# Optimization experiments

Measured on AMD Instinct MI355X. Metric: run time of the kernel, lower is better.

The kernel has to match this reference:

```python
import jax, jax.numpy as jnp
import numpy as np

A2B = 1.8897259886          # angstrom -> bohr
EV2HA = 0.0367493
NUM_RBF = 16
R_MIN = 0.5 * A2B
R_MAX = 4.0 * A2B           # r_max_angstroms=4.0 from gnn_config
RBF_WIDTH = (R_MAX - R_MIN) / NUM_RBF
N_NODES = 100_000
N_EDGES = 3_200_000
EMBED_DIM = 16
N_ELEMS = 4
CODES_PER_ELEM = 4          # all elements are core -> max_codes_per_element
TOTAL_CODES = N_ELEMS * CODES_PER_ELEM
NUM_PAIRS = 10
CODE_OWNER = np.repeat(np.arange(N_ELEMS), CODES_PER_ELEM)  # element owning each code


def setup_inputs() -> dict:
    key = jax.random.key(0)
    ks = jax.random.split(key, 12)
    N, E, D = N_NODES, N_EDGES, EMBED_DIM
    inv_sp = lambda v: np.float32(np.log(np.expm1(v)))  # inverse_softplus
    return {
        "elem_idx": jax.random.randint(ks[0], (N,), 0, N_ELEMS),
        "edge_index": jax.random.randint(ks[1], (2, E), 0, N),
        "distances": jax.random.uniform(ks[2], (E,), minval=1.0, maxval=7.5),  # bohr
        "pair_idx": jax.random.randint(ks[3], (E,), 0, NUM_PAIRS),
        "embed": jax.random.normal(ks[4], (N_ELEMS, D)),
        "fw1": jax.random.normal(ks[5], (D, NUM_RBF)) * 0.3,
        "fb1": jnp.zeros((D,)),
        "fw2": jax.random.normal(ks[6], (D, D)) * 0.3,
        "fb2": jnp.zeros((D,)),
        "mw1": jax.random.normal(ks[7], (D, D)) * 0.3,
        "mb1": jnp.zeros((D,)),
        "mw2": jax.random.normal(ks[8], (3, D)) * 0.05,  # zero-init in orig; small random for a live baseline
        "mb2": jnp.zeros((3,)),
        "codebook": jax.random.normal(ks[9], (TOTAL_CODES, D)),
        "raw_D_e": jnp.full((NUM_PAIRS,), inv_sp(0.1 * EV2HA)),
        "raw_alpha": jnp.full((NUM_PAIRS,), inv_sp(1.5 / A2B)),
        "raw_r0": jnp.full((NUM_PAIRS,), np.float32(3.0 * A2B)),
    }


def reference(elem_idx, edge_index, distances, pair_idx, embed,
              fw1, fb1, fw2, fb2, mw1, mb1, mw2, mb2,
              codebook, raw_D_e, raw_alpha, raw_r0):
    # --- EnvironmentEncoder: gather + edge filter + scatter_add ---
    h = embed[elem_idx]                                              # [N, D]
    centers = jnp.linspace(R_MIN, R_MAX, NUM_RBF, dtype=distances.dtype)
    rbf = jnp.exp(-0.5 * ((distances[:, None] - centers) / RBF_WIDTH) ** 2)  # [E, RBF]
    W = jax.nn.silu(rbf @ fw1.T + fb1) @ fw2.T + fb2                 # [E, D]
    src, tgt = edge_index[0], edge_index[1]
    messages = h[tgt] * W                                            # [E, D]
    agg = jax.ops.segment_sum(messages, src, num_segments=h.shape[0])
    h = h + agg                                                      # [N, D]

    # --- VectorQuantizer (eval path): per-element masked cdist + argmin ---
    d2 = (jnp.sum(h * h, axis=1, keepdims=True)
          - 2.0 * h @ codebook.T
          + jnp.sum(codebook * codebook, axis=1))                    # [N, C] squared dist
    owner = jnp.asarray(CODE_OWNER)
    valid = elem_idx[:, None] == owner[None, :]                      # [N, C]
    atom_types = jnp.argmin(jnp.where(valid, d2, jnp.inf), axis=1)   # [N]
    z_q = codebook[atom_types]                                       # [N, D]
    h_q = h + jax.lax.stop_gradient(z_q - h)                         # straight-through
    # all elements have >1 code -> commitment over all atoms
    vq_loss = 0.25 * jnp.mean((h - jax.lax.stop_gradient(z_q)) ** 2)

    # --- MorseParameterPredictor: edge gather + MLP ---
    pair_feat = h_q[src] + h_q[tgt]                                  # [E, D]
    delta = jax.nn.silu(pair_feat @ mw1.T + mb1) @ mw2.T + mb2       # [E, 3]

    D_e = jax.nn.softplus(raw_D_e[pair_idx] + delta[:, 0])
    alpha = jax.nn.softplus(raw_alpha[pair_idx] + delta[:, 1])
    r0 = raw_r0[pair_idx] + delta[:, 2]
    params = jnp.stack([D_e, alpha, r0], axis=-1)                    # [E, 3]
    return params, vq_loss
```

## Files before the change

### kernel.cpp

```cpp
#include <hip/hip_runtime.h>
#include <stdint.h>

#define A2B   1.8897259886f
#define R_MIN (0.5f * A2B)
#define R_MAX (4.0f * A2B)

#define EPB   2048
#define CSH   9

__global__ void __launch_bounds__(256) k_bucket(
        const int* __restrict__ src, const int* __restrict__ tgt,
        const int* __restrict__ elem, const float* __restrict__ dist,
        int* __restrict__ gCursor, float* __restrict__ dBuf,
        unsigned short* __restrict__ kBuf, int CAP, int E)
{
    __shared__ int cnt[4][256], sbase[4][256];
    int t = threadIdx.x;
    int w = t >> 6;
    cnt[0][t] = 0; cnt[1][t] = 0; cnt[2][t] = 0; cnt[3][t] = 0;
    __syncthreads();
    int e0 = blockIdx.x * EPB;
    int eEnd = (e0 + EPB < E) ? e0 + EPB : E;

    float dv[8]; int bv[8]; unsigned short kv[8];
    #pragma unroll
    for (int j = 0; j < 8; ++j) {
        int e = e0 + t + j * 256;
        if (e < eEnd) {
            int s = src[e];
            int q = elem[tgt[e]];
            dv[j] = dist[e];
            int b = s >> CSH;
            bv[j] = b;
            kv[j] = (unsigned short)(((s - (b << CSH)) << 2) | q);
            atomicAdd(&cnt[w][b], 1);
        }
    }
    __syncthreads();
    {
        int c0 = cnt[0][t], c1 = cnt[1][t], c2 = cnt[2][t], c3 = cnt[3][t];
        int tot = c0 + c1 + c2 + c3;
        int g = (tot > 0) ? atomicAdd(&gCursor[t], tot) : 0;
        sbase[0][t] = g;
        sbase[1][t] = g + c0;
        sbase[2][t] = g + c0 + c1;
        sbase[3][t] = g + c0 + c1 + c2;
        cnt[0][t] = 0; cnt[1][t] = 0; cnt[2][t] = 0; cnt[3][t] = 0;
    }
    __syncthreads();
    #pragma unroll
    for (int j = 0; j < 8; ++j) {
        int e = e0 + t + j * 256;
        if (e < eEnd) {
            int b = bv[j];
            int pos = sbase[w][b] + atomicAdd(&cnt[w][b], 1);
            if (pos < CAP) {
                size_t idx = (size_t)b * CAP + pos;
                dBuf[idx] = dv[j];
                kBuf[idx] = kv[j];
            }
        }
    }
}

__global__ void __launch_bounds__(256) k_bscan(
        const int* __restrict__ gCursor, int* __restrict__ bucketBase,
        int* __restrict__ offs, const float* __restrict__ fw1,
        float* __restrict__ fw1t, int NBUK, int N, int E)
{
    __shared__ int sd[256];
    int t = threadIdx.x;
    fw1t[t] = fw1[(t & 15) * 16 + (t >> 4)];
    int v = (t < NBUK) ? gCursor[t] : 0;
    sd[t] = v; __syncthreads();
    #pragma unroll
    for (int o = 1; o < 256; o <<= 1) {
        int x = (t >= o) ? sd[t - o] : 0;
        __syncthreads();
        sd[t] += x;
        __syncthreads();
    }
    bucketBase[t] = sd[t] - v;
    if (t == 0) offs[N] = E;
}

__global__ void __launch_bounds__(256) k_bin(
        const float* __restrict__ dBuf, const unsigned short* __restrict__ kBuf,
        const int* __restrict__ gCursor, const int* __restrict__ bucketBase,
        int* __restrict__ offs, float* __restrict__ payload,
        int CAP, int N)
{
    __shared__ int lcnt[512];
    __shared__ int sd[256];
    int t = threadIdx.x;
    int cb = blockIdx.x >> 2, fc = blockIdx.x & 3;
    int n0 = cb << CSH;
    int n1 = n0 + (1 << CSH); if (n1 > N) n1 = N;
    int m  = n1 - n0;
    int cntE = gCursor[cb]; if (cntE > CAP) cntE = CAP;
    int base = bucketBase[cb];
    lcnt[t] = 0; lcnt[t + 256] = 0;
    __syncthreads();
    const float* dB = dBuf + (size_t)cb * CAP;
    const unsigned short* kB = kBuf + (size_t)cb * CAP;
    for (int i = t; i < cntE; i += 256)
        atomicAdd(&lcnt[kB[i] >> 2], 1);
    __syncthreads();
    int b2 = t * 2;
    int v0 = (b2 < m)     ? lcnt[b2]     : 0;
    int v1 = (b2 + 1 < m) ? lcnt[b2 + 1] : 0;
    int tsum = v0 + v1;
    sd[t] = tsum; __syncthreads();
    #pragma unroll
    for (int o = 1; o < 256; o <<= 1) {
        int x = (t >= o) ? sd[t - o] : 0;
        __syncthreads();
        sd[t] += x;
        __syncthreads();
    }
    int run = sd[t] - tsum;
    if (b2 < m) {
        if ((b2 >> 7) == fc) offs[n0 + b2] = base + run;
        lcnt[b2] = run; run += v0;
    }
    if (b2 + 1 < m) {
        if (((b2 + 1) >> 7) == fc) offs[n0 + b2 + 1] = base + run;
        lcnt[b2 + 1] = run;
    }
    __syncthreads();
    for (int i = t; i < cntE; i += 256) {
        int kv = kB[i];
        int l = kv >> 2;
        if ((l >> 7) == fc) {
            int pos = atomicAdd(&lcnt[l], 1);
            unsigned db = __float_as_uint(dB[i]);
            payload[base + pos] = __uint_as_float((db & ~3u) | (unsigned)(kv & 3));
        }
    }
}

__global__ void __launch_bounds__(256) k_gather(
        const int* __restrict__ elem, const float* __restrict__ embed,
        const float* __restrict__ codebook,
        const float4* __restrict__ fw1t4, const float* __restrict__ fb1,
        const float* __restrict__ fw2, const float* __restrict__ fb2,
        const int* __restrict__ offs, const float* __restrict__ payload,
        int* __restrict__ atype, float* __restrict__ loss, int N)
{
    __shared__ float4 s_fw2v[64];
    __shared__ float s_cb[256];
    __shared__ float s_fb1[16], s_fb2[16], s_emb[64], s_cbn[16];
    __shared__ float s_red[4];
    __shared__ int s_ord[64];
    int t = threadIdx.x;
    {
        float* f2 = (float*)s_fw2v;
        f2[t] = fw2[t];
        s_cb[t] = codebook[t];
    }
    if (t < 16) { s_fb1[t] = fb1[t]; s_fb2[t] = fb2[t]; }
    if (t < 64) s_emb[t] = embed[t];
    int nbase = blockIdx.x * 64;
    if (t < 64) {
        int n = nbase + t;
        int dg = (n < N) ? (offs[n + 1] - offs[n]) : 0x7FFF;
        s_ord[t] = (dg << 6) | t;
    }
    __syncthreads();
    if (t < 16) {
        float s = 0.f;
        #pragma unroll
        for (int j = 0; j < 16; ++j) { float c = s_cb[t * 16 + j]; s += c * c; }
        s_cbn[t] = s;
    }
    for (int ksz = 2; ksz <= 64; ksz <<= 1) {
        for (int jj = ksz >> 1; jj > 0; jj >>= 1) {
            __syncthreads();
            if (t < 64) {
                int ixj = t ^ jj;
                if (ixj > t) {
                    int a = s_ord[t], b = s_ord[ixj];
                    bool asc = ((t & ksz) == 0);
                    if (asc ? (a > b) : (a < b)) { s_ord[t] = b; s_ord[ixj] = a; }
                }
            }
        }
    }
    __syncthreads();

    int node = nbase + (s_ord[t >> 2] & 63);
    int sub  = t & 3;
    float lp = 0.0f;
    if (node < N) {
        int o0 = offs[node], o1 = offs[node + 1];
        float G0[16], G1[16], G2[16], G3[16];
        #pragma unroll
        for (int j = 0; j < 16; ++j) { G0[j]=0.f; G1[j]=0.f; G2[j]=0.f; G3[j]=0.f; }
        float c0 = 0.f, c1 = 0.f, c2 = 0.f, c3 = 0.f;

        const float invw   = 16.0f / (R_MAX - R_MIN);
        const float u0base = R_MIN * invw;
        const float kstep  = 16.0f / 15.0f;
        for (int i = o0 + sub; i < o1; i += 8) {
            int ii = i + 4;
            bool has2 = (ii < o1);
            unsigned p0 = __float_as_uint(payload[i]);
            unsigned p1 = has2 ? __float_as_uint(payload[ii]) : p0;
            int q0 = (int)(p0 & 3u), q1 = (int)(p1 & 3u);
            float d0 = __uint_as_float(p0 & ~3u);
            float d1 = __uint_as_float(p1 & ~3u);
            float ua = d0 * invw - u0base;
            float ub = d1 * invw - u0base;
            float g0[16], g1[16];
            #pragma unroll
            for (int i2 = 0; i2 < 16; ++i2) { g0[i2] = s_fb1[i2]; g1[i2] = s_fb1[i2]; }
            #pragma clang loop unroll(disable)
            for (int k = 0; k < 16; ++k) {
                float r0 = __expf(-0.5f * ua * ua);
                float r1 = __expf(-0.5f * ub * ub);
                float4 w0 = fw1t4[k*4+0], w1 = fw1t4[k*4+1];
                float4 w2 = fw1t4[k*4+2], w3 = fw1t4[k*4+3];
                g0[0]+=r0*w0.x;  g0[1]+=r0*w0.y;  g0[2]+=r0*w0.z;  g0[3]+=r0*w0.w;
                g0[4]+=r0*w1.x;  g0[5]+=r0*w1.y;  g0[6]+=r0*w1.z;  g0[7]+=r0*w1.w;
                g0[8]+=r0*w2.x;  g0[9]+=r0*w2.y;  g0[10]+=r0*w2.z; g0[11]+=r0*w2.w;
                g0[12]+=r0*w3.x; g0[13]+=r0*w3.y; g0[14]+=r0*w3.z; g0[15]+=r0*w3.w;
                g1[0]+=r1*w0.x;  g1[1]+=r1*w0.y;  g1[2]+=r1*w0.z;  g1[3]+=r1*w0.w;
                g1[4]+=r1*w1.x;  g1[5]+=r1*w1.y;  g1[6]+=r1*w1.z;  g1[7]+=r1*w1.w;
                g1[8]+=r1*w2.x;  g1[9]+=r1*w2.y;  g1[10]+=r1*w2.z; g1[11]+=r1*w2.w;
                g1[12]+=r1*w3.x; g1[13]+=r1*w3.y; g1[14]+=r1*w3.z; g1[15]+=r1*w3.w;
                ua -= kstep; ub -= kstep;
            }
            {
                float m0 = (q0==0)?1.f:0.f, m1 = (q0==1)?1.f:0.f;
                float m2 = (q0==2)?1.f:0.f, m3 = (q0==3)?1.f:0.f;
                c0 += m0; c1 += m1; c2 += m2; c3 += m3;
                #pragma unroll
                for (int i2 = 0; i2 < 16; ++i2) {
                    float a = g0[i2];
                    float s = a * __builtin_amdgcn_rcpf(1.0f + __expf(-a));
                    G0[i2] += m0*s; G1[i2] += m1*s; G2[i2] += m2*s; G3[i2] += m3*s;
                }
            }
            if (has2) {
                float m0 = (q1==0)?1.f:0.f, m1 = (q1==1)?1.f:0.f;
                float m2 = (q1==2)?1.f:0.f, m3 = (q1==3)?1.f:0.f;
                c0 += m0; c1 += m1; c2 += m2; c3 += m3;
                #pragma unroll
                for (int i2 = 0; i2 < 16; ++i2) {
                    float a = g1[i2];
                    float s = a * __builtin_amdgcn_rcpf(1.0f + __expf(-a));
                    G0[i2] += m0*s; G1[i2] += m1*s; G2[i2] += m2*s; G3[i2] += m3*s;
                }
            }
        }
        #pragma unroll
        for (int mm = 1; mm <= 2; mm <<= 1) {
            #pragma unroll
            for (int j = 0; j < 16; ++j) {
                G0[j] += __shfl_xor(G0[j], mm, 64);
                G1[j] += __shfl_xor(G1[j], mm, 64);
                G2[j] += __shfl_xor(G2[j], mm, 64);
                G3[j] += __shfl_xor(G3[j], mm, 64);
            }
            c0 += __shfl_xor(c0, mm, 64);
            c1 += __shfl_xor(c1, mm, 64);
            c2 += __shfl_xor(c2, mm, 64);
            c3 += __shfl_xor(c3, mm, 64);
        }
        float Gs[16];
        #pragma unroll
        for (int j = 0; j < 16; ++j)
            Gs[j] = (sub==0) ? G0[j] : (sub==1) ? G1[j] : (sub==2) ? G2[j] : G3[j];
        float cs = (sub==0) ? c0 : (sub==1) ? c1 : (sub==2) ? c2 : c3;
        const float* er = s_emb + sub * 16;
        float acc[16];
        #pragma clang loop unroll_count(4)
        for (int j = 0; j < 16; ++j) {
            float4 f0 = s_fw2v[j*4+0], f1 = s_fw2v[j*4+1];
            float4 f2 = s_fw2v[j*4+2], f3 = s_fw2v[j*4+3];
            float w = Gs[0]*f0.x  + Gs[1]*f0.y  + Gs[2]*f0.z  + Gs[3]*f0.w
                    + Gs[4]*f1.x  + Gs[5]*f1.y  + Gs[6]*f1.z  + Gs[7]*f1.w
                    + Gs[8]*f2.x  + Gs[9]*f2.y  + Gs[10]*f2.z + Gs[11]*f2.w
                    + Gs[12]*f3.x + Gs[13]*f3.y + Gs[14]*f3.z + Gs[15]*f3.w;
            acc[j] = (w + cs * s_fb2[j]) * er[j];
        }
        #pragma unroll
        for (int mm = 1; mm <= 2; mm <<= 1) {
            #pragma unroll
            for (int j = 0; j < 16; ++j)
                acc[j] += __shfl_xor(acc[j], mm, 64);
        }
        int qn = elem[node];
        float h[16], hh = 0.f;
        #pragma unroll
        for (int j = 0; j < 16; ++j) {
            h[j] = acc[j] + s_emb[qn * 16 + j];
            hh += h[j] * h[j];
        }
        float best = __builtin_inff(); int bi = 0;
        #pragma unroll
        for (int c = 0; c < 4; ++c) {
            int code = qn * 4 + c;
            float dot = 0.f;
            #pragma unroll
            for (int j = 0; j < 16; ++j) dot += h[j] * s_cb[code * 16 + j];
            float d2 = hh - 2.0f * dot + s_cbn[code];
            if (d2 < best) { best = d2; bi = code; }
        }
        if (sub == 0) {
            atype[node] = bi;
            #pragma unroll
            for (int j = 0; j < 16; ++j) {
                float df = h[j] - s_cb[bi * 16 + j];
                lp += df * df;
            }
        }
    }
    #pragma unroll
    for (int o = 32; o > 0; o >>= 1) lp += __shfl_down(lp, o, 64);
    int wid = t >> 6;
    if ((t & 63) == 0) s_red[wid] = lp;
    __syncthreads();
    if (t == 0) atomicAdd(loss, s_red[0] + s_red[1] + s_red[2] + s_red[3]);
}

__global__ void __launch_bounds__(256) k_table(
        const float* __restrict__ codebook,
        const float* __restrict__ mw1, const float* __restrict__ mb1,
        const float* __restrict__ mw2, const float* __restrict__ mb2,
        const float* __restrict__ rD, const float* __restrict__ rA,
        const float* __restrict__ rR,
        const float* __restrict__ loss, float4* __restrict__ table,
        float* __restrict__ out_loss, float inv_nd)
{
    __shared__ float s_cb[256], s_mw1[256], s_mb1[16], s_mw2[48], s_mb2[3];
    __shared__ float s_rd[10], s_ra[10], s_rr[10];
    int tid = threadIdx.x;
    s_cb[tid] = codebook[tid];
    s_mw1[tid] = mw1[tid];
    if (tid < 16) s_mb1[tid] = mb1[tid];
    if (tid < 48) s_mw2[tid] = mw2[tid];
    if (tid < 3)  s_mb2[tid] = mb2[tid];
    if (tid < 10) { s_rd[tid] = rD[tid]; s_ra[tid] = rA[tid]; s_rr[tid] = rR[tid]; }
    __syncthreads();

    int a = tid >> 4, b = tid & 15;
    float pf[16];
    #pragma unroll
    for (int j = 0; j < 16; ++j) pf[j] = s_cb[a * 16 + j] + s_cb[b * 16 + j];
    float hid[16];
    #pragma unroll
    for (int i = 0; i < 16; ++i) {
        float acc = s_mb1[i];
        #pragma unroll
        for (int j = 0; j < 16; ++j) acc += pf[j] * s_mw1[i * 16 + j];
        hid[i] = acc / (1.0f + __expf(-acc));
    }
    float del[3];
    #pragma unroll
    for (int r = 0; r < 3; ++r) {
        float acc = s_mb2[r];
        #pragma unroll
        for (int i = 0; i < 16; ++i) acc += hid[i] * s_mw2[r * 16 + i];
        del[r] = acc;
    }
    #pragma unroll
    for (int p = 0; p < 10; ++p) {
        float xd = s_rd[p] + del[0];
        float xa = s_ra[p] + del[1];
        float De = (xd > 20.f) ? xd : log1pf(__expf(xd));
        float al = (xa > 20.f) ? xa : log1pf(__expf(xa));
        float r0 = s_rr[p] + del[2];
        table[tid * 10 + p] = make_float4(De, al, r0, 0.f);
    }
    if (tid == 0) out_loss[0] = 0.25f * loss[0] * inv_nd;
}

__global__ void __launch_bounds__(256) k_out(
        const int* __restrict__ src, const int* __restrict__ tgt,
        const int* __restrict__ pidx, const int* __restrict__ atype,
        const float4* __restrict__ table, float2* __restrict__ out, int Ehalf)
{
    int i = blockIdx.x * 256 + threadIdx.x;
    if (i >= Ehalf) return;
    int2 s2 = ((const int2*)src)[i];
    int2 t2 = ((const int2*)tgt)[i];
    int2 p2 = ((const int2*)pidx)[i];
    int i0 = (atype[s2.x] * 16 + atype[t2.x]) * 10 + p2.x;
    int i1 = (atype[s2.y] * 16 + atype[t2.y]) * 10 + p2.y;
    float4 t0 = table[i0];
    float4 t1 = table[i1];
    float2* op = out + (size_t)3 * i;
    op[0] = make_float2(t0.x, t0.y);
    op[1] = make_float2(t0.z, t1.x);
    op[2] = make_float2(t1.y, t1.z);
}

extern "C" void kernel_launch(void* const* d_in, const int* in_sizes, int n_in,
                              void* d_out, int out_size, void* d_ws, size_t ws_size,
                              hipStream_t stream)
{
    (void)n_in;
    const int*   elem  = (const int*)d_in[0];
    const int*   eidx  = (const int*)d_in[1];
    const float* dist  = (const float*)d_in[2];
    const int*   pidx  = (const int*)d_in[3];
    const float* embed = (const float*)d_in[4];
    const float* fw1   = (const float*)d_in[5];
    const float* fb1   = (const float*)d_in[6];
    const float* fw2   = (const float*)d_in[7];
    const float* fb2   = (const float*)d_in[8];
    const float* mw1   = (const float*)d_in[9];
    const float* mb1   = (const float*)d_in[10];
    const float* mw2   = (const float*)d_in[11];
    const float* mb2   = (const float*)d_in[12];
    const float* cb    = (const float*)d_in[13];
    const float* rD    = (const float*)d_in[14];
    const float* rA    = (const float*)d_in[15];
    const float* rR    = (const float*)d_in[16];

    int N = in_sizes[0];
    int E = in_sizes[2];
    const int* src = eidx;
    const int* tgt = eidx + E;

    int NBUK = (N + (1 << CSH) - 1) >> CSH;
    if (NBUK > 256) return;
    long long expv = ((long long)E << CSH) / N;
    int CAP = (int)(expv + expv / 16 + 256);

    size_t outBytes = (size_t)out_size * 4;
    char* ob = (char*)d_out;
    size_t oc = 0;
    float* dBuf = (float*)(ob + oc);           oc += (size_t)NBUK * CAP * 4;
    unsigned short* kBuf = (unsigned short*)(ob + oc); oc += (size_t)NBUK * CAP * 2;
    oc = (oc + 3) & ~(size_t)3;
    float* payload = (float*)(ob + oc);        oc += (size_t)E * 4;
    int*   offs    = (int*)(ob + oc);          oc += (size_t)(N + 1) * 4;
    if (oc > outBytes) return;

    char* ws = (char*)d_ws;
    size_t cur = 0;
    int*   gCursor    = (int*)(ws + cur);  cur += 256 * 4;
    float* loss       = (float*)(ws + cur); cur += 4;
    size_t clearB = cur;
    cur = (cur + 15) & ~(size_t)15;
    int*   bucketBase = (int*)(ws + cur);  cur += 256 * 4;
    float* fw1t       = (float*)(ws + cur); cur += 256 * 4;
    int*   atype      = (int*)(ws + cur);  cur += (size_t)N * 4;
    cur = (cur + 15) & ~(size_t)15;
    float4* table     = (float4*)(ws + cur); cur += 2560 * sizeof(float4);
    if (ws_size < cur) return;

    hipMemsetAsync(d_ws, 0, clearB, stream);

    k_bucket<<<(E + EPB - 1) / EPB, 256, 0, stream>>>(
        src, tgt, elem, dist, gCursor, dBuf, kBuf, CAP, E);
    k_bscan<<<1, 256, 0, stream>>>(gCursor, bucketBase, offs, fw1, fw1t,
                                   NBUK, N, E);
    k_bin<<<NBUK * 4, 256, 0, stream>>>(dBuf, kBuf, gCursor, bucketBase,
                                        offs, payload, CAP, N);
    k_gather<<<(N + 63) / 64, 256, 0, stream>>>(elem, embed, cb,
                                                (const float4*)fw1t, fb1,
                                                fw2, fb2, offs, payload,
                                                atype, loss, N);
    float* outl = (float*)d_out + (size_t)3 * E;
    k_table<<<1, 256, 0, stream>>>(cb, mw1, mb1, mw2, mb2, rD, rA, rR,
                                   loss, table, outl,
                                   1.0f / (float)((size_t)N * 16));
    k_out<<<(E / 2 + 255) / 256, 256, 0, stream>>>(src, tgt, pidx, atype, table,
                                                   (float2*)d_out, E / 2);
}
```

Before: 263.8 us.

## Fold bucket scan into binning kernel and quantize edge-filter accumulators to integers

Removes the single-block scan kernel: the weight transpose moves into the bucketing kernel, and each binning block recomputes the bucket prefix sum itself. Binning now uses two blocks per bucket instead of four. The gather kernel accumulates SiLU outputs as fixed-point integers with select-add instead of float mask multiplies. The goal is fewer launches and cheaper masked accumulation, at the cost of quantization error and redundant scans.

```diff
diff --git a/kernel.cpp b/kernel.cpp
--- a/kernel.cpp
+++ b/kernel.cpp
@@ -7,16 +7,21 @@
 
 #define EPB   2048
 #define CSH   9
+#define QSCALE 1048576.0f
+#define QINV   (1.0f / 1048576.0f)
 
 __global__ void __launch_bounds__(256) k_bucket(
         const int* __restrict__ src, const int* __restrict__ tgt,
         const int* __restrict__ elem, const float* __restrict__ dist,
+        const float* __restrict__ fw1, float* __restrict__ fw1t,
         int* __restrict__ gCursor, float* __restrict__ dBuf,
         unsigned short* __restrict__ kBuf, int CAP, int E)
 {
     __shared__ int cnt[4][256], sbase[4][256];
     int t = threadIdx.x;
     int w = t >> 6;
+    if (blockIdx.x == 0)
+        fw1t[t] = fw1[(t & 15) * 16 + (t >> 4)];
     cnt[0][t] = 0; cnt[1][t] = 0; cnt[2][t] = 0; cnt[3][t] = 0;
     __syncthreads();
     int e0 = blockIdx.x * EPB;
@@ -63,14 +68,17 @@
     }
 }
 
-__global__ void __launch_bounds__(256) k_bscan(
-        const int* __restrict__ gCursor, int* __restrict__ bucketBase,
-        int* __restrict__ offs, const float* __restrict__ fw1,
-        float* __restrict__ fw1t, int NBUK, int N, int E)
-{
+__global__ void __launch_bounds__(256) k_bin(
+        const float* __restrict__ dBuf, const unsigned short* __restrict__ kBuf,
+        const int* __restrict__ gCursor, int* __restrict__ offs,
+        float* __restrict__ payload, int CAP, int NBUK, int N, int E)
+{
+    __shared__ int lcnt[512];
     __shared__ int sd[256];
+    __shared__ int s_base;
     int t = threadIdx.x;
-    fw1t[t] = fw1[(t & 15) * 16 + (t >> 4)];
+    int cb = blockIdx.x >> 1, fc = blockIdx.x & 1;
+    lcnt[t] = 0; lcnt[t + 256] = 0;
     int v = (t < NBUK) ? gCursor[t] : 0;
     sd[t] = v; __syncthreads();
     #pragma unroll
@@ -80,27 +88,16 @@
         sd[t] += x;
         __syncthreads();
     }
-    bucketBase[t] = sd[t] - v;
-    if (t == 0) offs[N] = E;
-}
-
-__global__ void __launch_bounds__(256) k_bin(
-        const float* __restrict__ dBuf, const unsigned short* __restrict__ kBuf,
-        const int* __restrict__ gCursor, const int* __restrict__ bucketBase,
-        int* __restrict__ offs, float* __restrict__ payload,
-        int CAP, int N)
-{
-    __shared__ int lcnt[512];
-    __shared__ int sd[256];
-    int t = threadIdx.x;
-    int cb = blockIdx.x >> 2, fc = blockIdx.x & 3;
+    if (t == cb) s_base = sd[t] - v;
+    __syncthreads();
+    int base = s_base;
+
     int n0 = cb << CSH;
     int n1 = n0 + (1 << CSH); if (n1 > N) n1 = N;
     int m  = n1 - n0;
     int cntE = gCursor[cb]; if (cntE > CAP) cntE = CAP;
-    int base = bucketBase[cb];
-    lcnt[t] = 0; lcnt[t + 256] = 0;
-    __syncthreads();
+    if (cb == 0 && fc == 0 && t == 0) offs[N] = E;
+
     const float* dB = dBuf + (size_t)cb * CAP;
     const unsigned short* kB = kBuf + (size_t)cb * CAP;
     for (int i = t; i < cntE; i += 256)
@@ -120,18 +117,18 @@
     }
     int run = sd[t] - tsum;
     if (b2 < m) {
-        if ((b2 >> 7) == fc) offs[n0 + b2] = base + run;
+        if ((b2 >> 8) == fc) offs[n0 + b2] = base + run;
         lcnt[b2] = run; run += v0;
     }
     if (b2 + 1 < m) {
-        if (((b2 + 1) >> 7) == fc) offs[n0 + b2 + 1] = base + run;
+        if (((b2 + 1) >> 8) == fc) offs[n0 + b2 + 1] = base + run;
         lcnt[b2 + 1] = run;
     }
     __syncthreads();
     for (int i = t; i < cntE; i += 256) {
         int kv = kB[i];
         int l = kv >> 2;
-        if ((l >> 7) == fc) {
+        if ((l >> 8) == fc) {
             int pos = atomicAdd(&lcnt[l], 1);
             unsigned db = __float_as_uint(dB[i]);
             payload[base + pos] = __uint_as_float((db & ~3u) | (unsigned)(kv & 3));
@@ -193,10 +190,10 @@
     float lp = 0.0f;
     if (node < N) {
         int o0 = offs[node], o1 = offs[node + 1];
-        float G0[16], G1[16], G2[16], G3[16];
-        #pragma unroll
-        for (int j = 0; j < 16; ++j) { G0[j]=0.f; G1[j]=0.f; G2[j]=0.f; G3[j]=0.f; }
-        float c0 = 0.f, c1 = 0.f, c2 = 0.f, c3 = 0.f;
+        int G0[16], G1[16], G2[16], G3[16];
+        #pragma unroll
+        for (int j = 0; j < 16; ++j) { G0[j]=0; G1[j]=0; G2[j]=0; G3[j]=0; }
+        int c0 = 0, c1 = 0, c2 = 0, c3 = 0;
 
         const float invw   = 16.0f / (R_MAX - R_MIN);
         const float u0base = R_MIN * invw;
@@ -231,25 +228,29 @@
                 ua -= kstep; ub -= kstep;
             }
             {
-                float m0 = (q0==0)?1.f:0.f, m1 = (q0==1)?1.f:0.f;
-                float m2 = (q0==2)?1.f:0.f, m3 = (q0==3)?1.f:0.f;
-                c0 += m0; c1 += m1; c2 += m2; c3 += m3;
+                c0 += (q0==0); c1 += (q0==1); c2 += (q0==2); c3 += (q0==3);
                 #pragma unroll
                 for (int i2 = 0; i2 < 16; ++i2) {
                     float a = g0[i2];
                     float s = a * __builtin_amdgcn_rcpf(1.0f + __expf(-a));
-                    G0[i2] += m0*s; G1[i2] += m1*s; G2[i2] += m2*s; G3[i2] += m3*s;
+                    int sq = __float2int_rn(s * QSCALE);
+                    G0[i2] += (q0==0) ? sq : 0;
+                    G1[i2] += (q0==1) ? sq : 0;
+                    G2[i2] += (q0==2) ? sq : 0;
+                    G3[i2] += (q0==3) ? sq : 0;
                 }
             }
             if (has2) {
-                float m0 = (q1==0)?1.f:0.f, m1 = (q1==1)?1.f:0.f;
-                float m2 = (q1==2)?1.f:0.f, m3 = (q1==3)?1.f:0.f;
-                c0 += m0; c1 += m1; c2 += m2; c3 += m3;
+                c0 += (q1==0); c1 += (q1==1); c2 += (q1==2); c3 += (q1==3);
                 #pragma unroll
                 for (int i2 = 0; i2 < 16; ++i2) {
                     float a = g1[i2];
                     float s = a * __builtin_amdgcn_rcpf(1.0f + __expf(-a));
-                    G0[i2] += m0*s; G1[i2] += m1*s; G2[i2] += m2*s; G3[i2] += m3*s;
+                    int sq = __float2int_rn(s * QSCALE);
+                    G0[i2] += (q1==0) ? sq : 0;
+                    G1[i2] += (q1==1) ? sq : 0;
+                    G2[i2] += (q1==2) ? sq : 0;
+                    G3[i2] += (q1==3) ? sq : 0;
                 }
             }
         }
@@ -269,9 +270,11 @@
         }
         float Gs[16];
         #pragma unroll
-        for (int j = 0; j < 16; ++j)
-            Gs[j] = (sub==0) ? G0[j] : (sub==1) ? G1[j] : (sub==2) ? G2[j] : G3[j];
-        float cs = (sub==0) ? c0 : (sub==1) ? c1 : (sub==2) ? c2 : c3;
+        for (int j = 0; j < 16; ++j) {
+            int gq = (sub==0) ? G0[j] : (sub==1) ? G1[j] : (sub==2) ? G2[j] : G3[j];
+            Gs[j] = (float)gq * QINV;
+        }
+        float cs = (float)((sub==0) ? c0 : (sub==1) ? c1 : (sub==2) ? c2 : c3);
         const float* er = s_emb + sub * 16;
         float acc[16];
         #pragma clang loop unroll_count(4)
@@ -441,25 +444,22 @@
 
     char* ws = (char*)d_ws;
     size_t cur = 0;
-    int*   gCursor    = (int*)(ws + cur);  cur += 256 * 4;
-    float* loss       = (float*)(ws + cur); cur += 4;
+    int*   gCursor = (int*)(ws + cur);  cur += 256 * 4;
+    float* loss    = (float*)(ws + cur); cur += 4;
     size_t clearB = cur;
     cur = (cur + 15) & ~(size_t)15;
-    int*   bucketBase = (int*)(ws + cur);  cur += 256 * 4;
-    float* fw1t       = (float*)(ws + cur); cur += 256 * 4;
-    int*   atype      = (int*)(ws + cur);  cur += (size_t)N * 4;
+    float* fw1t    = (float*)(ws + cur); cur += 256 * 4;
+    int*   atype   = (int*)(ws + cur);  cur += (size_t)N * 4;
     cur = (cur + 15) & ~(size_t)15;
-    float4* table     = (float4*)(ws + cur); cur += 2560 * sizeof(float4);
+    float4* table  = (float4*)(ws + cur); cur += 2560 * sizeof(float4);
     if (ws_size < cur) return;
 
     hipMemsetAsync(d_ws, 0, clearB, stream);
 
     k_bucket<<<(E + EPB - 1) / EPB, 256, 0, stream>>>(
-        src, tgt, elem, dist, gCursor, dBuf, kBuf, CAP, E);
-    k_bscan<<<1, 256, 0, stream>>>(gCursor, bucketBase, offs, fw1, fw1t,
-                                   NBUK, N, E);
-    k_bin<<<NBUK * 4, 256, 0, stream>>>(dBuf, kBuf, gCursor, bucketBase,
-                                        offs, payload, CAP, N);
+        src, tgt, elem, dist, fw1, fw1t, gCursor, dBuf, kBuf, CAP, E);
+    k_bin<<<NBUK * 2, 256, 0, stream>>>(dBuf, kBuf, gCursor, offs, payload,
+                                        CAP, NBUK, N, E);
     k_gather<<<(N + 63) / 64, 256, 0, stream>>>(elem, embed, cb,
                                                 (const float4*)fw1t, fb1,
                                                 fw2, fb2, offs, payload,
```

Result: slower. 274.0 us (+3.9%).
